# Kernel optimization log

Measured on AMD Instinct MI355X. Metric: run time of the kernel, lower is better.

## Reference

```python
import jax, jax.numpy as jnp
import numpy as np
import math

B, S, D, H = 4, 2048, 1024, 16
HD = D // H  # 64
SCALE = math.sqrt(HD)  # scale=True -> sqrt(d_model // n_head)

def setup_inputs() -> dict:
    key = jax.random.key(0)
    k1, k2, k3, k4, k5 = jax.random.split(key, 5)
    x = jax.random.normal(k1, (B, S, D), dtype=jnp.float32)
    char_ids = jax.random.randint(k2, (B, S), 0, 21128)
    seq_len = jax.random.randint(k3, (B,), 1, S)
    mask = jnp.ones((B, S), dtype=jnp.int64)
    W_qkv = jax.random.normal(k4, (D, 3 * D), dtype=jnp.float32) * (1.0 / math.sqrt(D))
    W_fc = jax.random.normal(k5, (D, D), dtype=jnp.float32) * (1.0 / math.sqrt(D))
    b_fc = jnp.zeros((D,), dtype=jnp.float32)
    return {"x": x, "char_ids": char_ids, "seq_len": seq_len, "mask": mask,
            "W_qkv": W_qkv, "W_fc": W_fc, "b_fc": b_fc}

def reference(x, char_ids, seq_len, mask, W_qkv, W_fc, b_fc):
    b, s, d = x.shape
    qkv = x @ W_qkv                      # [b, s, 3d]
    q, k, v = jnp.split(qkv, 3, axis=-1)
    # [b, h, s, hd]
    q = q.reshape(b, s, H, HD).transpose(0, 2, 1, 3)
    k = k.reshape(b, s, H, HD).transpose(0, 2, 1, 3)
    v = v.reshape(b, s, H, HD).transpose(0, 2, 1, 3)
    attn = jnp.einsum('bhqd,bhkd->bhqk', q, k) / SCALE
    attn = jnp.where(mask[:, None, None, :] == 0, -jnp.inf, attn)
    attn = jax.nn.softmax(attn, axis=-1)
    # dropout is identity in eval mode
    out = jnp.einsum('bhqk,bhkd->bhqd', attn, v)
    out = out.transpose(0, 2, 1, 3).reshape(b, s, d)
    return out @ W_fc + b_fc
```

## Files before the change

kernel.cpp:

```cpp
#include <hip/hip_runtime.h>
#include <hip/hip_bf16.h>


#define S_ 2048
#define D_ 1024

typedef __attribute__((ext_vector_type(4))) float f32x4;
typedef __attribute__((ext_vector_type(16))) float f32x16;
typedef __attribute__((ext_vector_type(8))) short bf16x8;

__device__ __forceinline__ unsigned short f2b(float f) {
  union { float f; unsigned u; } x; x.f = f;
  unsigned r = x.u + 0x7fffu + ((x.u >> 16) & 1u);
  return (unsigned short)(r >> 16);
}
__device__ __forceinline__ float b2f(unsigned short u) {
  union { unsigned u; float f; } x; x.u = ((unsigned)u) << 16; return x.f;
}

__device__ __forceinline__ void gload_lds16(const void* g, void* l) {
  __builtin_amdgcn_global_load_lds(
      (const __attribute__((address_space(1))) unsigned int*)g,
      (__attribute__((address_space(3))) unsigned int*)l, 16, 0, 0);
}

__global__ void cvt_f32_bf16(const float* __restrict__ in, unsigned short* __restrict__ out, int n) {
  int i = (blockIdx.x * blockDim.x + threadIdx.x) * 8;
  if (i >= n) return;
  float4 a = *(const float4*)&in[i];
  float4 b = *(const float4*)&in[i + 4];
  unsigned short r[8];
  r[0] = f2b(a.x); r[1] = f2b(a.y); r[2] = f2b(a.z); r[3] = f2b(a.w);
  r[4] = f2b(b.x); r[5] = f2b(b.y); r[6] = f2b(b.z); r[7] = f2b(b.w);
  *(uint4*)&out[i] = *(uint4*)r;
}

__global__ void transpose_cvt(const float* __restrict__ W, unsigned short* __restrict__ Wt,
                              int K, int N) {
  __shared__ unsigned short tile[32][33];
  int n0 = blockIdx.x * 32, k0 = blockIdx.y * 32;
  int tx = threadIdx.x & 31, ty = threadIdx.x >> 5;
  #pragma unroll
  for (int i = 0; i < 32; i += 8)
    tile[ty + i][tx] = f2b(W[(size_t)(k0 + ty + i) * N + n0 + tx]);
  __syncthreads();
  #pragma unroll
  for (int i = 0; i < 32; i += 8)
    Wt[(size_t)(n0 + ty + i) * K + k0 + tx] = tile[tx][ty + i];
}

__global__ __launch_bounds__(256) void gemm_bt(const unsigned short* __restrict__ A,
                                               const unsigned short* __restrict__ Bt,
                                               const float* __restrict__ bias,
                                               float* __restrict__ Cf,
                                               unsigned short* __restrict__ Cb,
                                               int M, int N, int K) {
  __shared__ unsigned short As[128 * 32];
  __shared__ unsigned short Bs[128 * 32];
  int tid = threadIdx.x, wave = tid >> 6, lane = tid & 63;
  int bm = blockIdx.x, bn = blockIdx.y;
  int wr = (wave >> 1) * 64, wc = (wave & 1) * 64;
  f32x4 acc[4][4] = {};

  const unsigned short* aG0 = A + (size_t)(bm * 128 + wave * 32 + (lane >> 2)) * K + (lane & 3) * 8;
  const unsigned short* aG1 = aG0 + (size_t)16 * K;
  const unsigned short* bG0 = Bt + (size_t)(bn * 128 + wave * 32 + (lane >> 2)) * K + (lane & 3) * 8;
  const unsigned short* bG1 = bG0 + (size_t)16 * K;
  unsigned short* aL0 = As + wave * 32 * 32;
  unsigned short* aL1 = aL0 + 16 * 32;
  unsigned short* bL0 = Bs + wave * 32 * 32;
  unsigned short* bL1 = bL0 + 16 * 32;

  for (int k0 = 0; k0 < K; k0 += 32) {
    gload_lds16(aG0, aL0); gload_lds16(aG1, aL1);
    gload_lds16(bG0, bL0); gload_lds16(bG1, bL1);
    aG0 += 32; aG1 += 32; bG0 += 32; bG1 += 32;
    __syncthreads();
    bf16x8 af[4], bf[4];
    #pragma unroll
    for (int i = 0; i < 4; i++)
      af[i] = *(const bf16x8*)&As[(wr + i * 16 + (lane & 15)) * 32 + (lane >> 4) * 8];
    #pragma unroll
    for (int i = 0; i < 4; i++)
      bf[i] = *(const bf16x8*)&Bs[(wc + i * 16 + (lane & 15)) * 32 + (lane >> 4) * 8];
    #pragma unroll
    for (int i = 0; i < 4; i++)
      #pragma unroll
      for (int j = 0; j < 4; j++)
        acc[i][j] = __builtin_amdgcn_mfma_f32_16x16x32_bf16(af[i], bf[j], acc[i][j], 0, 0, 0);
    __syncthreads();
  }

  int row0 = bm * 128 + wr + (lane >> 4) * 4;
  int col0 = bn * 128 + wc + (lane & 15);
  if (Cb) {
    #pragma unroll
    for (int i = 0; i < 4; i++)
      #pragma unroll
      for (int j = 0; j < 4; j++)
        #pragma unroll
        for (int q = 0; q < 4; q++)
          Cb[(size_t)(row0 + i * 16 + q) * N + col0 + j * 16] = f2b(acc[i][j][q]);
  } else {
    #pragma unroll
    for (int i = 0; i < 4; i++)
      #pragma unroll
      for (int j = 0; j < 4; j++) {
        float bv = bias[col0 + j * 16];
        #pragma unroll
        for (int q = 0; q < 4; q++)
          Cf[(size_t)(row0 + i * 16 + q) * N + col0 + j * 16] = acc[i][j][q] + bv;
      }
  }
}

__global__ __launch_bounds__(256) void flash_attn(const unsigned short* __restrict__ qkv,
                                                  unsigned short* __restrict__ ao) {
  __shared__ unsigned short Ks[2][4096];
  __shared__ unsigned short Vs[2][4096];
  int tid = threadIdx.x, wave = tid >> 6, lane = tid & 63;
  int l31 = lane & 31, hi = lane >> 5;
  int bh = blockIdx.y, b = bh >> 4, h = bh & 15;
  const unsigned short* base = qkv + (size_t)b * S_ * 3072 + h * 64;
  const unsigned short* kb = base + 1024;
  const unsigned short* vb = base + 2048;
  int q0 = blockIdx.x * 128 + wave * 32;

  bf16x8 qf[4];
  {
    const unsigned short* qp = base + (size_t)(q0 + l31) * 3072 + hi * 8;
    #pragma unroll
    for (int ks = 0; ks < 4; ks++) {
      bf16x8 v = *(const bf16x8*)(qp + ks * 16);
      #pragma unroll
      for (int e = 0; e < 8; e++) v[e] = (short)f2b(0.125f * b2f((unsigned short)v[e]));
      qf[ks] = v;
    }
  }

  f32x16 o0 = {}, o1 = {};
  float mi = -1e30f, li = 0.f;

  int r_l = lane >> 3;
  int gsrc = (lane & 7) ^ r_l;
  size_t koffA = (size_t)((wave * 2 + 0) * 8 + r_l) * 3072 + gsrc * 8;
  size_t koffB = (size_t)((wave * 2 + 1) * 8 + r_l) * 3072 + gsrc * 8;
  int kvv = tid & 63, dgr = (tid >> 6) * 16;
  bf16x8 vr0, vr1;

  {
    gload_lds16(kb + koffA, &Ks[0][(wave * 2 + 0) * 512]);
    gload_lds16(kb + koffB, &Ks[0][(wave * 2 + 1) * 512]);
    const unsigned short* vsrc = vb + (size_t)kvv * 3072 + dgr;
    vr0 = *(const bf16x8*)vsrc;
    vr1 = *(const bf16x8*)(vsrc + 8);
    #pragma unroll
    for (int e = 0; e < 16; e++) {
      int d = dgr + e;
      Vs[0][d * 64 + ((((kvv >> 3) ^ (d & 7)) << 3)) + (kvv & 7)] =
          (unsigned short)(e < 8 ? vr0[e] : vr1[e - 8]);
    }
    __syncthreads();
  }

  for (int t = 0; t < 32; ++t) {
    int cur = t & 1;
    int tn = (t + 1) & 31;
    {
      const unsigned short* ksrc = kb + (size_t)tn * 64 * 3072;
      gload_lds16(ksrc + koffA, &Ks[cur ^ 1][(wave * 2 + 0) * 512]);
      gload_lds16(ksrc + koffB, &Ks[cur ^ 1][(wave * 2 + 1) * 512]);
      const unsigned short* vsrc = vb + (size_t)(tn * 64 + kvv) * 3072 + dgr;
      vr0 = *(const bf16x8*)vsrc;
      vr1 = *(const bf16x8*)(vsrc + 8);
    }

    const unsigned short* Kc = Ks[cur];
    const unsigned short* Vc = Vs[cur];

    #pragma unroll
    for (int sub = 0; sub < 2; ++sub) {
      f32x16 sA = {};
      #pragma unroll
      for (int ks = 0; ks < 4; ks++) {
        int row = sub * 32 + l31;
        bf16x8 kf = *(const bf16x8*)&Kc[row * 64 + ((((ks << 1) + hi) ^ (row & 7)) << 3)];
        sA = __builtin_amdgcn_mfma_f32_32x32x16_bf16(kf, qf[ks], sA, 0, 0, 0);
      }

      float m0 = fmaxf(sA[0], sA[1]),  m1 = fmaxf(sA[2], sA[3]);
      float m2 = fmaxf(sA[4], sA[5]),  m3 = fmaxf(sA[6], sA[7]);
      float m4 = fmaxf(sA[8], sA[9]),  m5 = fmaxf(sA[10], sA[11]);
      float m6 = fmaxf(sA[12], sA[13]), m7 = fmaxf(sA[14], sA[15]);
      m0 = fmaxf(m0, m1); m2 = fmaxf(m2, m3); m4 = fmaxf(m4, m5); m6 = fmaxf(m6, m7);
      float tm = fmaxf(fmaxf(m0, m2), fmaxf(m4, m6));
      tm = fmaxf(tm, __shfl_xor(tm, 32, 64));
      if (__any(tm > mi + 8.f)) {
        float tnew = fmaxf(mi, tm);
        float fac = __expf(mi - tnew);
        li *= fac; mi = tnew;
        #pragma unroll
        for (int r = 0; r < 16; r++) { o0[r] *= fac; o1[r] *= fac; }
      }
      float p[16];
      float rs = 0.f;
      #pragma unroll
      for (int r = 0; r < 16; r++) { p[r] = __expf(sA[r] - mi); rs += p[r]; }
      rs += __shfl_xor(rs, 32, 64);
      li += rs;

      unsigned c0, c1, c2, c3, c4, c5, c6, c7;
      asm("v_cvt_pk_bf16_f32 %0, %1, %2" : "=v"(c0) : "v"(p[0]),  "v"(p[1]));
      asm("v_cvt_pk_bf16_f32 %0, %1, %2" : "=v"(c1) : "v"(p[2]),  "v"(p[3]));
      asm("v_cvt_pk_bf16_f32 %0, %1, %2" : "=v"(c2) : "v"(p[4]),  "v"(p[5]));
      asm("v_cvt_pk_bf16_f32 %0, %1, %2" : "=v"(c3) : "v"(p[6]),  "v"(p[7]));
      asm("v_cvt_pk_bf16_f32 %0, %1, %2" : "=v"(c4) : "v"(p[8]),  "v"(p[9]));
      asm("v_cvt_pk_bf16_f32 %0, %1, %2" : "=v"(c5) : "v"(p[10]), "v"(p[11]));
      asm("v_cvt_pk_bf16_f32 %0, %1, %2" : "=v"(c6) : "v"(p[12]), "v"(p[13]));
      asm("v_cvt_pk_bf16_f32 %0, %1, %2" : "=v"(c7) : "v"(p[14]), "v"(p[15]));
      asm volatile("v_permlane32_swap_b32 %0, %1" : "+v"(c0), "+v"(c2));
      asm volatile("v_permlane32_swap_b32 %0, %1" : "+v"(c1), "+v"(c3));
      asm volatile("v_permlane32_swap_b32 %0, %1" : "+v"(c4), "+v"(c6));
      asm volatile("v_permlane32_swap_b32 %0, %1" : "+v"(c5), "+v"(c7));
      union { unsigned u[4]; bf16x8 v; } P0, P1;
      P0.u[0] = c0; P0.u[1] = c1; P0.u[2] = c2; P0.u[3] = c3;
      P1.u[0] = c4; P1.u[1] = c5; P1.u[2] = c6; P1.u[3] = c7;

      #pragma unroll
      for (int ks2 = 0; ks2 < 2; ks2++) {
        bf16x8 pf = ks2 ? P1.v : P0.v;
        int slot = (sub << 2) + (ks2 << 1) + hi;
        bf16x8 vf0 = *(const bf16x8*)&Vc[l31 * 64 + ((slot ^ (l31 & 7)) << 3)];
        bf16x8 vf1 = *(const bf16x8*)&Vc[(32 + l31) * 64 + ((slot ^ (l31 & 7)) << 3)];
        o0 = __builtin_amdgcn_mfma_f32_32x32x16_bf16(vf0, pf, o0, 0, 0, 0);
        o1 = __builtin_amdgcn_mfma_f32_32x32x16_bf16(vf1, pf, o1, 0, 0, 0);
      }
    }

    {
      unsigned short* Vd = Vs[cur ^ 1];
      #pragma unroll
      for (int e = 0; e < 16; e++) {
        int d = dgr + e;
        Vd[d * 64 + ((((kvv >> 3) ^ (d & 7)) << 3)) + (kvv & 7)] =
            (unsigned short)(e < 8 ? vr0[e] : vr1[e - 8]);
      }
    }
    __syncthreads();
  }

  float inv = 1.f / li;
  unsigned short* aop = ao + (size_t)(b * S_ + q0 + l31) * D_ + h * 64;
  #pragma unroll
  for (int g = 0; g < 4; g++) {
    union { unsigned short s[4]; uint2 u; } w0, w1;
    #pragma unroll
    for (int e = 0; e < 4; e++) {
      w0.s[e] = f2b(o0[g * 4 + e] * inv);
      w1.s[e] = f2b(o1[g * 4 + e] * inv);
    }
    int d = g * 8 + hi * 4;
    *(uint2*)&aop[d] = w0.u;
    *(uint2*)&aop[32 + d] = w1.u;
  }
}

extern "C" void kernel_launch(void* const* d_in, const int* in_sizes, int n_in,
                              void* d_out, int out_size, void* d_ws, size_t ws_size,
                              hipStream_t stream) {
  const float* x    = (const float*)d_in[0];
  const float* Wqkv = (const float*)d_in[4];
  const float* Wfc  = (const float*)d_in[5];
  const float* bfc  = (const float*)d_in[6];
  float* out = (float*)d_out;

  char* ws = (char*)d_ws;
  unsigned short* xb    = (unsigned short*)(ws);
  unsigned short* qkv   = (unsigned short*)(ws + 16777216);
  unsigned short* ao    = (unsigned short*)(ws + 67108864);
  unsigned short* wqkvT = (unsigned short*)(ws + 83886080);
  unsigned short* wfcT  = (unsigned short*)(ws + 90177536);

  cvt_f32_bf16<<<dim3(4096), dim3(256), 0, stream>>>(x, xb, 8388608);
  transpose_cvt<<<dim3(96, 32), dim3(256), 0, stream>>>(Wqkv, wqkvT, 1024, 3072);
  transpose_cvt<<<dim3(32, 32), dim3(256), 0, stream>>>(Wfc, wfcT, 1024, 1024);
  gemm_bt<<<dim3(64, 24), dim3(256), 0, stream>>>(xb, wqkvT, nullptr, nullptr, qkv, 8192, 3072, 1024);
  flash_attn<<<dim3(16, 64), dim3(256), 0, stream>>>(qkv, ao);
  gemm_bt<<<dim3(64, 8), dim3(256), 0, stream>>>(ao, wfcT, bfc, out, nullptr, 8192, 1024, 1024);
}
```

Before: 249.1 us.

## Split PV accumulators, add MFMA priority hints, and swap attention grid axes

The attention kernel now keeps two independent pairs of output accumulators, so the two PV MFMA chains no longer depend on each other. It also loads all four V fragments before issuing the MFMAs and wraps the MFMA sections in s_setprio to raise wave priority. The row-sum cross-lane shuffle moves out of the loop to one final reduction, and the max tree is restructured. The grid axes are swapped so consecutive blocks cover different heads rather than different query tiles, which changes L2 locality; the extra accumulators raise register pressure.

```diff
diff --git a/kernel.cpp b/kernel.cpp
--- a/kernel.cpp
+++ b/kernel.cpp
@@ -120,11 +120,11 @@
   __shared__ unsigned short Vs[2][4096];
   int tid = threadIdx.x, wave = tid >> 6, lane = tid & 63;
   int l31 = lane & 31, hi = lane >> 5;
-  int bh = blockIdx.y, b = bh >> 4, h = bh & 15;
+  int bh = blockIdx.x, b = bh >> 4, h = bh & 15;
   const unsigned short* base = qkv + (size_t)b * S_ * 3072 + h * 64;
   const unsigned short* kb = base + 1024;
   const unsigned short* vb = base + 2048;
-  int q0 = blockIdx.x * 128 + wave * 32;
+  int q0 = blockIdx.y * 128 + wave * 32;
 
   bf16x8 qf[4];
   {
@@ -138,7 +138,7 @@
     }
   }
 
-  f32x16 o0 = {}, o1 = {};
+  f32x16 o0a = {}, o0b = {}, o1a = {}, o1b = {};
   float mi = -1e30f, li = 0.f;
 
   int r_l = lane >> 3;
@@ -181,32 +181,35 @@
     #pragma unroll
     for (int sub = 0; sub < 2; ++sub) {
       f32x16 sA = {};
+      __builtin_amdgcn_s_setprio(1);
       #pragma unroll
       for (int ks = 0; ks < 4; ks++) {
         int row = sub * 32 + l31;
         bf16x8 kf = *(const bf16x8*)&Kc[row * 64 + ((((ks << 1) + hi) ^ (row & 7)) << 3)];
         sA = __builtin_amdgcn_mfma_f32_32x32x16_bf16(kf, qf[ks], sA, 0, 0, 0);
       }
-
-      float m0 = fmaxf(sA[0], sA[1]),  m1 = fmaxf(sA[2], sA[3]);
-      float m2 = fmaxf(sA[4], sA[5]),  m3 = fmaxf(sA[6], sA[7]);
-      float m4 = fmaxf(sA[8], sA[9]),  m5 = fmaxf(sA[10], sA[11]);
-      float m6 = fmaxf(sA[12], sA[13]), m7 = fmaxf(sA[14], sA[15]);
-      m0 = fmaxf(m0, m1); m2 = fmaxf(m2, m3); m4 = fmaxf(m4, m5); m6 = fmaxf(m6, m7);
-      float tm = fmaxf(fmaxf(m0, m2), fmaxf(m4, m6));
+      __builtin_amdgcn_s_setprio(0);
+
+      float t0 = fmaxf(fmaxf(sA[0], sA[1]), sA[2]);
+      float t1 = fmaxf(fmaxf(sA[3], sA[4]), sA[5]);
+      float t2 = fmaxf(fmaxf(sA[6], sA[7]), sA[8]);
+      float t3 = fmaxf(fmaxf(sA[9], sA[10]), sA[11]);
+      float t4 = fmaxf(fmaxf(sA[12], sA[13]), sA[14]);
+      float tm = fmaxf(fmaxf(fmaxf(t0, t1), t2), fmaxf(fmaxf(t3, t4), sA[15]));
       tm = fmaxf(tm, __shfl_xor(tm, 32, 64));
       if (__any(tm > mi + 8.f)) {
         float tnew = fmaxf(mi, tm);
         float fac = __expf(mi - tnew);
         li *= fac; mi = tnew;
         #pragma unroll
-        for (int r = 0; r < 16; r++) { o0[r] *= fac; o1[r] *= fac; }
+        for (int r = 0; r < 16; r++) {
+          o0a[r] *= fac; o0b[r] *= fac; o1a[r] *= fac; o1b[r] *= fac;
+        }
       }
       float p[16];
       float rs = 0.f;
       #pragma unroll
       for (int r = 0; r < 16; r++) { p[r] = __expf(sA[r] - mi); rs += p[r]; }
-      rs += __shfl_xor(rs, 32, 64);
       li += rs;
 
       unsigned c0, c1, c2, c3, c4, c5, c6, c7;
@@ -226,15 +229,18 @@
       P0.u[0] = c0; P0.u[1] = c1; P0.u[2] = c2; P0.u[3] = c3;
       P1.u[0] = c4; P1.u[1] = c5; P1.u[2] = c6; P1.u[3] = c7;
 
-      #pragma unroll
-      for (int ks2 = 0; ks2 < 2; ks2++) {
-        bf16x8 pf = ks2 ? P1.v : P0.v;
-        int slot = (sub << 2) + (ks2 << 1) + hi;
-        bf16x8 vf0 = *(const bf16x8*)&Vc[l31 * 64 + ((slot ^ (l31 & 7)) << 3)];
-        bf16x8 vf1 = *(const bf16x8*)&Vc[(32 + l31) * 64 + ((slot ^ (l31 & 7)) << 3)];
-        o0 = __builtin_amdgcn_mfma_f32_32x32x16_bf16(vf0, pf, o0, 0, 0, 0);
-        o1 = __builtin_amdgcn_mfma_f32_32x32x16_bf16(vf1, pf, o1, 0, 0, 0);
-      }
+      int slot0 = (sub << 2) + hi;
+      int slot1 = (sub << 2) + 2 + hi;
+      bf16x8 vA0 = *(const bf16x8*)&Vc[l31 * 64 + ((slot0 ^ (l31 & 7)) << 3)];
+      bf16x8 vA1 = *(const bf16x8*)&Vc[(32 + l31) * 64 + ((slot0 ^ (l31 & 7)) << 3)];
+      bf16x8 vB0 = *(const bf16x8*)&Vc[l31 * 64 + ((slot1 ^ (l31 & 7)) << 3)];
+      bf16x8 vB1 = *(const bf16x8*)&Vc[(32 + l31) * 64 + ((slot1 ^ (l31 & 7)) << 3)];
+      __builtin_amdgcn_s_setprio(1);
+      o0a = __builtin_amdgcn_mfma_f32_32x32x16_bf16(vA0, P0.v, o0a, 0, 0, 0);
+      o1a = __builtin_amdgcn_mfma_f32_32x32x16_bf16(vA1, P0.v, o1a, 0, 0, 0);
+      o0b = __builtin_amdgcn_mfma_f32_32x32x16_bf16(vB0, P1.v, o0b, 0, 0, 0);
+      o1b = __builtin_amdgcn_mfma_f32_32x32x16_bf16(vB1, P1.v, o1b, 0, 0, 0);
+      __builtin_amdgcn_s_setprio(0);
     }
 
     {
@@ -249,6 +255,7 @@
     __syncthreads();
   }
 
+  li += __shfl_xor(li, 32, 64);
   float inv = 1.f / li;
   unsigned short* aop = ao + (size_t)(b * S_ + q0 + l31) * D_ + h * 64;
   #pragma unroll
@@ -256,8 +263,8 @@
     union { unsigned short s[4]; uint2 u; } w0, w1;
     #pragma unroll
     for (int e = 0; e < 4; e++) {
-      w0.s[e] = f2b(o0[g * 4 + e] * inv);
-      w1.s[e] = f2b(o1[g * 4 + e] * inv);
+      w0.s[e] = f2b((o0a[g * 4 + e] + o0b[g * 4 + e]) * inv);
+      w1.s[e] = f2b((o1a[g * 4 + e] + o1b[g * 4 + e]) * inv);
     }
     int d = g * 8 + hi * 4;
     *(uint2*)&aop[d] = w0.u;
@@ -285,6 +292,6 @@
   transpose_cvt<<<dim3(96, 32), dim3(256), 0, stream>>>(Wqkv, wqkvT, 1024, 3072);
   transpose_cvt<<<dim3(32, 32), dim3(256), 0, stream>>>(Wfc, wfcT, 1024, 1024);
   gemm_bt<<<dim3(64, 24), dim3(256), 0, stream>>>(xb, wqkvT, nullptr, nullptr, qkv, 8192, 3072, 1024);
-  flash_attn<<<dim3(16, 64), dim3(256), 0, stream>>>(qkv, ao);
+  flash_attn<<<dim3(64, 16), dim3(256), 0, stream>>>(qkv, ao);
   gemm_bt<<<dim3(64, 8), dim3(256), 0, stream>>>(ao, wfcT, bfc, out, nullptr, 8192, 1024, 1024);
 }
```

Result: faster. 237.3 us (-4.8%).
